# Kernel optimization log

Hardware: AMD Instinct MI355X
Metric: run time of the kernel (lower is better)

## Reference

```python
import jax, jax.numpy as jnp
import numpy as np

N, E = 50000, 800000
C, H, EC = 64, 3, 32  # node_channels, heads, edge_channels
NEG_SLOPE = 0.2


def _kaiming(key, shape, fan_in):
    bound = np.sqrt(6.0 / fan_in)  # kaiming_uniform_ default (a=sqrt(5)-ish approx; gain sqrt(2) variant)
    return jax.random.uniform(key, shape, jnp.float32, -bound, bound)


def setup_inputs() -> dict:
    key = jax.random.key(0)
    ks = jax.random.split(key, 8)
    x = jax.random.normal(ks[0], (N, C), jnp.float32)
    edge_index = jax.random.randint(ks[1], (2, E), 0, N, jnp.int64)
    edge_attr = jax.random.normal(ks[2], (E, EC), jnp.float32)
    weight_node = _kaiming(ks[3], (C, H * C), C)
    weight_edge = _kaiming(ks[4], (EC, H * C), EC)
    weight_triplet_att = _kaiming(ks[5], (1, H, 3 * C), 3 * C)
    weight_scale = _kaiming(ks[6], (H * C, C), H * C)
    bias = jnp.zeros((C,), jnp.float32)
    return {"x": x, "edge_index": edge_index, "edge_attr": edge_attr,
            "weight_node": weight_node, "weight_edge": weight_edge,
            "weight_triplet_att": weight_triplet_att,
            "weight_scale": weight_scale, "bias": bias}


def reference(x, edge_index, edge_attr, weight_node, weight_edge,
              weight_triplet_att, weight_scale, bias):
    src = edge_index[0]  # j (source)
    dst = edge_index[1]  # i (target), PyG default flow source_to_target

    xp = x @ weight_node                     # [N, H*C]
    ep = edge_attr @ weight_edge             # [E, H*C]

    x_j = xp[src].reshape(E, H, C)
    x_i = xp[dst].reshape(E, H, C)
    e_ij = ep.reshape(E, H, C)

    # attention weight split along concat order [x_i, e_ij, x_j]
    w = weight_triplet_att.reshape(H, 3, C)
    alpha = (jnp.einsum('ehc,hc->eh', x_i, w[:, 0])
             + jnp.einsum('ehc,hc->eh', e_ij, w[:, 1])
             + jnp.einsum('ehc,hc->eh', x_j, w[:, 2]))   # [E, H]
    alpha = jnp.where(alpha >= 0, alpha, NEG_SLOPE * alpha)  # leaky_relu

    # segment softmax over destination nodes (PyG softmax semantics)
    seg_max = jax.ops.segment_max(alpha, dst, num_segments=N)    # [N, H]
    alpha = jnp.exp(alpha - seg_max[dst])
    seg_sum = jax.ops.segment_sum(alpha, dst, num_segments=N)    # [N, H]
    alpha = alpha / (seg_sum[dst] + 1e-16)

    msg = alpha[:, :, None] * e_ij * x_j                         # [E, H, C]
    aggr = jax.ops.segment_sum(msg.reshape(E, H * C), dst, num_segments=N)  # [N, H*C]

    return aggr @ weight_scale + bias                            # [N, C]
```

## Files before the change

### kernel.cpp

```cpp
#include <hip/hip_runtime.h>

#define CC    64
#define HH    3
#define ECC   32
#define HCdim 192
#define NEG_SLOPE 0.2f
#define ASHIFT 12.0f
#define LOG2E  1.44269504f

typedef float v2f __attribute__((ext_vector_type(2)));

__global__ void tm_k0(const float* __restrict__ We, const float* __restrict__ wt,
                      float* __restrict__ u) {
    int t = threadIdx.x;
    if (t >= HH * ECC) return;
    int h = t >> 5, k = t & 31;
    float s = 0.f;
    #pragma unroll
    for (int c = 0; c < CC; ++c)
        s = fmaf(We[k * HCdim + h * CC + c], wt[h * HCdim + CC + c], s);
    u[t] = s;
}

#define K1_ROWS 64
__global__ __launch_bounds__(192) void tm_k1(const float* __restrict__ x,
        const float* __restrict__ Wn, const float* __restrict__ wt,
        const int* __restrict__ ei, int* __restrict__ deg,
        _Float16* __restrict__ xp16, float* __restrict__ sA, int N, int E) {
    __shared__ float wl[CC * HCdim];
    __shared__ float xl[K1_ROWS * CC];
    const int t = threadIdx.x;
    for (int i = blockIdx.x * 192 + t; i < E; i += gridDim.x * 192)
        atomicAdd(&deg[ei[E + i]], 1);
    const int h = t >> 6, c = t & 63;
    {
        float4* wl4 = (float4*)wl;
        const float4* Wn4 = (const float4*)Wn;
        for (int i = t; i < CC * HCdim / 4; i += 192) wl4[i] = Wn4[i];
    }
    const int base = blockIdx.x * K1_ROWS;
    const int rows = min(K1_ROWS, N - base);
    {
        float4* xl4 = (float4*)xl;
        const float4* x4 = (const float4*)(x + (size_t)base * CC);
        for (int i = t; i < rows * CC / 4; i += 192) xl4[i] = x4[i];
    }
    const float w0c = wt[h * HCdim + c];
    const float w2c = wt[h * HCdim + 2 * CC + c];
    __syncthreads();
    for (int rt = 0; rt < rows; rt += 4) {
        float acc0 = 0.f, acc1 = 0.f, acc2 = 0.f, acc3 = 0.f;
        #pragma unroll 4
        for (int k = 0; k < CC; k += 4) {
            const float w0  = wl[(k + 0) * HCdim + t];
            const float w1  = wl[(k + 1) * HCdim + t];
            const float w2_ = wl[(k + 2) * HCdim + t];
            const float w3  = wl[(k + 3) * HCdim + t];
            const float4 xa = *(const float4*)&xl[(rt + 0) * CC + k];
            const float4 xb = *(const float4*)&xl[(rt + 1) * CC + k];
            const float4 xc = *(const float4*)&xl[(rt + 2) * CC + k];
            const float4 xd = *(const float4*)&xl[(rt + 3) * CC + k];
            acc0 = fmaf(xa.x, w0, fmaf(xa.y, w1, fmaf(xa.z, w2_, fmaf(xa.w, w3, acc0))));
            acc1 = fmaf(xb.x, w0, fmaf(xb.y, w1, fmaf(xb.z, w2_, fmaf(xb.w, w3, acc1))));
            acc2 = fmaf(xc.x, w0, fmaf(xc.y, w1, fmaf(xc.z, w2_, fmaf(xc.w, w3, acc2))));
            acc3 = fmaf(xd.x, w0, fmaf(xd.y, w1, fmaf(xd.z, w2_, fmaf(xd.w, w3, acc3))));
        }
        #pragma unroll
        for (int r = 0; r < 4; ++r) {
            const float v = (r == 0) ? acc0 : (r == 1) ? acc1 : (r == 2) ? acc2 : acc3;
            const int n = base + rt + r;
            xp16[(size_t)n * HCdim + t] = (_Float16)v;
            float a0 = v * w0c, a2 = v * w2c;
            #pragma unroll
            for (int o = 32; o; o >>= 1) {
                a0 += __shfl_xor(a0, o);
                a2 += __shfl_xor(a2, o);
            }
            if (c == 0) {
                sA[n * 8 + h]     = a0;
                sA[n * 8 + 4 + h] = a2;
            }
        }
    }
}

__global__ __launch_bounds__(256) void tm_scanA(const int* __restrict__ deg,
        int* __restrict__ bsum, int N) {
    __shared__ int sd[256];
    int t = threadIdx.x, n = blockIdx.x * 256 + t;
    sd[t] = (n < N) ? deg[n] : 0;
    __syncthreads();
    for (int o = 128; o; o >>= 1) {
        if (t < o) sd[t] += sd[t + o];
        __syncthreads();
    }
    if (!t) bsum[blockIdx.x] = sd[0];
}

__global__ __launch_bounds__(256) void tm_scanB(const int* __restrict__ bsum,
        int* __restrict__ boff, int nb) {
    __shared__ int sd[256];
    int t = threadIdx.x;
    int v = (t < nb) ? bsum[t] : 0;
    sd[t] = v;
    __syncthreads();
    for (int o = 1; o < 256; o <<= 1) {
        int x = (t >= o) ? sd[t - o] : 0;
        __syncthreads();
        sd[t] += x;
        __syncthreads();
    }
    if (t < nb) boff[t] = sd[t] - v;
}

__global__ __launch_bounds__(256) void tm_scanC(const int* __restrict__ deg,
        const int* __restrict__ boff, int* __restrict__ off,
        int* __restrict__ cursor, int N) {
    __shared__ int sd[256];
    int t = threadIdx.x, n = blockIdx.x * 256 + t;
    int v = (n < N) ? deg[n] : 0;
    sd[t] = v;
    __syncthreads();
    for (int o = 1; o < 256; o <<= 1) {
        int x = (t >= o) ? sd[t - o] : 0;
        __syncthreads();
        sd[t] += x;
        __syncthreads();
    }
    if (n < N) {
        int ex = boff[blockIdx.x] + sd[t] - v;
        off[n] = ex;
        cursor[n] = ex;
        if (n == N - 1) off[N] = ex + v;
    }
}

__global__ __launch_bounds__(256) void tm_alpha(const int* __restrict__ ei,
        const float* __restrict__ ea, const float* __restrict__ u,
        const float* __restrict__ sA, int* __restrict__ cursor,
        float4* __restrict__ alphaE, int2* __restrict__ perm, int E) {
    __shared__ float ul[HH * ECC];
    const int t = threadIdx.x;
    if (t < HH * ECC) ul[t] = u[t];
    __syncthreads();
    const int e = blockIdx.x * 256 + t;
    if (e >= E) return;
    const int src = ei[e];
    const int dst = ei[E + e];
    float av[ECC];
    const float4* p4 = (const float4*)(ea + (size_t)e * ECC);
    #pragma unroll
    for (int q = 0; q < 8; ++q) {
        float4 v = p4[q];
        av[4*q] = v.x; av[4*q+1] = v.y; av[4*q+2] = v.z; av[4*q+3] = v.w;
    }
    float d0 = 0.f, d1 = 0.f, d2 = 0.f;
    #pragma unroll
    for (int k = 0; k < ECC; ++k) {
        d0 = fmaf(av[k], ul[k], d0);
        d1 = fmaf(av[k], ul[ECC + k], d1);
        d2 = fmaf(av[k], ul[2 * ECC + k], d2);
    }
    const float4 s0 = *(const float4*)(sA + (size_t)dst * 8);
    const float4 s2 = *(const float4*)(sA + (size_t)src * 8 + 4);
    float a0 = s0.x + d0 + s2.x;
    float a1 = s0.y + d1 + s2.y;
    float a2 = s0.z + d2 + s2.z;
    a0 = (a0 >= 0.f) ? a0 : NEG_SLOPE * a0;
    a1 = (a1 >= 0.f) ? a1 : NEG_SLOPE * a1;
    a2 = (a2 >= 0.f) ? a2 : NEG_SLOPE * a2;
    alphaE[e] = make_float4((a0 - ASHIFT) * LOG2E,
                            (a1 - ASHIFT) * LOG2E,
                            (a2 - ASHIFT) * LOG2E, 0.f);
    const int pos = atomicAdd(&cursor[dst], 1);
    perm[pos] = make_int2(src * (HCdim * 2), e * (ECC * 4));
}

__global__ __launch_bounds__(192) void tm_agg(const int2* __restrict__ perm,
        const int* __restrict__ off, const float* __restrict__ ea,
        const float* __restrict__ We, const float* __restrict__ alphaE,
        const _Float16* __restrict__ xp16, float* __restrict__ aggrN, int N) {
    const int t = threadIdx.x;
    const int h = t >> 6, lane = t & 63;
    const char* __restrict__ ea_b = (const char*)ea;
    const char* __restrict__ xp_b = (const char*)xp16;
    const char* __restrict__ al_b = (const char*)alphaE;
    v2f wcol2[16];
    #pragma unroll
    for (int k2 = 0; k2 < 16; ++k2) {
        wcol2[k2].x = We[(2 * k2)     * HCdim + h * CC + lane];
        wcol2[k2].y = We[(2 * k2 + 1) * HCdim + h * CC + lane];
    }
    const int xoff = h * (CC * 2) + lane * 2;
    const int aoff = h * 4;
    for (int n = blockIdx.x; n < N; n += gridDim.x) {
        const int start = off[n], end = off[n + 1];
        float s = 0.f, acc = 0.f;
        int pos = start;
        int4 pp = (pos + 2 <= end) ? *(const int4*)&perm[pos]
                                   : make_int4(0, 0, 0, 0);
        for (; pos + 2 <= end; ) {
            const int4 cur = pp;
            pos += 2;
            if (pos + 2 <= end) pp = *(const int4*)&perm[pos];
            const int so0 = __builtin_amdgcn_readfirstlane(cur.x);
            const int eo0 = __builtin_amdgcn_readfirstlane(cur.y);
            const int so1 = __builtin_amdgcn_readfirstlane(cur.z);
            const int eo1 = __builtin_amdgcn_readfirstlane(cur.w);
            const float a0 = *(const float*)(al_b + (eo0 >> 3) + aoff);
            const float a1 = *(const float*)(al_b + (eo1 >> 3) + aoff);
            const float4* q0 = (const float4*)(ea_b + eo0);
            const float4* q1 = (const float4*)(ea_b + eo1);
            const float xj0 = (float)*(const _Float16*)(xp_b + so0 + xoff);
            const float xj1 = (float)*(const _Float16*)(xp_b + so1 + xoff);
            v2f d0 = {0.f, 0.f}, d1 = {0.f, 0.f};
            #pragma unroll
            for (int q = 0; q < 8; ++q) {
                const float4 v0 = q0[q];
                const float4 v1 = q1[q];
                const v2f wlo = wcol2[2 * q], whi = wcol2[2 * q + 1];
                d0 = (v2f){v0.x, v0.y} * wlo + d0;
                d0 = (v2f){v0.z, v0.w} * whi + d0;
                d1 = (v2f){v1.x, v1.y} * wlo + d1;
                d1 = (v2f){v1.z, v1.w} * whi + d1;
            }
            const float p0 = exp2f(a0);
            const float p1 = exp2f(a1);
            s += p0 + p1;
            acc = fmaf(p0 * (d0.x + d0.y), xj0, acc);
            acc = fmaf(p1 * (d1.x + d1.y), xj1, acc);
        }
        if (pos < end) {
            const int2 pe = perm[pos];
            const int so = __builtin_amdgcn_readfirstlane(pe.x);
            const int eo = __builtin_amdgcn_readfirstlane(pe.y);
            const float a = *(const float*)(al_b + (eo >> 3) + aoff);
            const float4* q4 = (const float4*)(ea_b + eo);
            const float xj = (float)*(const _Float16*)(xp_b + so + xoff);
            v2f d = {0.f, 0.f};
            #pragma unroll
            for (int q = 0; q < 8; ++q) {
                const float4 v = q4[q];
                d = (v2f){v.x, v.y} * wcol2[2 * q]     + d;
                d = (v2f){v.z, v.w} * wcol2[2 * q + 1] + d;
            }
            const float p = exp2f(a);
            s += p;
            acc = fmaf(p * (d.x + d.y), xj, acc);
        }
        aggrN[(size_t)n * HCdim + h * CC + lane] = acc / (s + 1e-16f);
    }
}

#define K5_ROWS 16
__global__ __launch_bounds__(256) void tm_k5(const float* __restrict__ aggrN,
        const float* __restrict__ Ws, const float* __restrict__ bias,
        float* __restrict__ out, int N) {
    __shared__ float wsl[HCdim * CC];
    __shared__ float al[K5_ROWS * HCdim];
    const int t = threadIdx.x;
    const int part = t >> 6, c = t & 63;
    {
        float4* w4 = (float4*)wsl;
        const float4* Ws4 = (const float4*)Ws;
        for (int i = t; i < HCdim * CC / 4; i += 256) w4[i] = Ws4[i];
    }
    const float b = bias[c];
    const int base = blockIdx.x * K5_ROWS;
    const int rows = min(K5_ROWS, N - base);
    {
        float4* al4 = (float4*)al;
        const float4* a4 = (const float4*)(aggrN + (size_t)base * HCdim);
        for (int i = t; i < rows * HCdim / 4; i += 256) al4[i] = a4[i];
    }
    __syncthreads();
    const int r0 = part * 4;
    if (r0 >= rows) return;
    float acc0 = b, acc1 = b, acc2 = b, acc3 = b;
    #pragma unroll 4
    for (int k = 0; k < HCdim; k += 4) {
        const float w0  = wsl[(k + 0) * CC + c];
        const float w1  = wsl[(k + 1) * CC + c];
        const float w2_ = wsl[(k + 2) * CC + c];
        const float w3  = wsl[(k + 3) * CC + c];
        const float4 xa = *(const float4*)&al[(r0 + 0) * HCdim + k];
        const float4 xb = *(const float4*)&al[(r0 + 1) * HCdim + k];
        const float4 xc = *(const float4*)&al[(r0 + 2) * HCdim + k];
        const float4 xd = *(const float4*)&al[(r0 + 3) * HCdim + k];
        acc0 = fmaf(xa.x, w0, fmaf(xa.y, w1, fmaf(xa.z, w2_, fmaf(xa.w, w3, acc0))));
        acc1 = fmaf(xb.x, w0, fmaf(xb.y, w1, fmaf(xb.z, w2_, fmaf(xb.w, w3, acc1))));
        acc2 = fmaf(xc.x, w0, fmaf(xc.y, w1, fmaf(xc.z, w2_, fmaf(xc.w, w3, acc2))));
        acc3 = fmaf(xd.x, w0, fmaf(xd.y, w1, fmaf(xd.z, w2_, fmaf(xd.w, w3, acc3))));
    }
    if (r0 + 0 < rows) out[(size_t)(base + r0 + 0) * CC + c] = acc0;
    if (r0 + 1 < rows) out[(size_t)(base + r0 + 1) * CC + c] = acc1;
    if (r0 + 2 < rows) out[(size_t)(base + r0 + 2) * CC + c] = acc2;
    if (r0 + 3 < rows) out[(size_t)(base + r0 + 3) * CC + c] = acc3;
}

extern "C" void kernel_launch(void* const* d_in, const int* in_sizes, int n_in,
                              void* d_out, int out_size, void* d_ws, size_t ws_size,
                              hipStream_t stream) {
    const float* x    = (const float*)d_in[0];
    const int*   ei   = (const int*)d_in[1];
    const float* ea   = (const float*)d_in[2];
    const float* Wn   = (const float*)d_in[3];
    const float* We   = (const float*)d_in[4];
    const float* wt   = (const float*)d_in[5];
    const float* Ws   = (const float*)d_in[6];
    const float* bias = (const float*)d_in[7];
    float* out = (float*)d_out;
    const int N = in_sizes[0] / CC;
    const int E = in_sizes[1] / 2;
    const int nb = (N + 255) / 256;

    float* ws = (float*)d_ws;
    size_t o = 0;
    _Float16* xp16 = (_Float16*)(ws + o); o += (size_t)N * HCdim / 2;
    float* sA = ws + o;                  o += (size_t)N * 8;
    float* u  = ws + o;                  o += 128;
    float4* alphaE = (float4*)(ws + o);  o += (size_t)E * 4;
    int2*  perm = (int2*)(ws + o);       o += (size_t)E * 2 + 32;
    int* deg    = (int*)(ws + o);        o += N;
    int* off    = (int*)(ws + o);        o += N + 1;
    int* cursor = (int*)(ws + o);        o += N;
    int* bsum   = (int*)(ws + o);        o += 256;
    int* boff   = (int*)(ws + o);        o += 256;
    o += (4 - (o & 3)) & 3;
    float* aggrN = ws + o;               o += (size_t)N * HCdim;
    (void)ws_size; (void)n_in; (void)out_size;

    (void)hipMemsetAsync(deg, 0, (size_t)N * sizeof(int), stream);

    tm_k0<<<1, 96, 0, stream>>>(We, wt, u);
    tm_k1<<<(N + K1_ROWS - 1) / K1_ROWS, 192, 0, stream>>>(x, Wn, wt, ei, deg,
                                                           xp16, sA, N, E);
    tm_scanA<<<nb, 256, 0, stream>>>(deg, bsum, N);
    tm_scanB<<<1, 256, 0, stream>>>(bsum, boff, nb);
    tm_scanC<<<nb, 256, 0, stream>>>(deg, boff, off, cursor, N);
    tm_alpha<<<(E + 255) / 256, 256, 0, stream>>>(ei, ea, u, sA, cursor,
                                                  alphaE, perm, E);
    tm_agg<<<(N + 7) / 8, 192, 0, stream>>>(perm, off, ea, We,
                                            (const float*)alphaE, xp16, aggrN, N);
    tm_k5<<<(N + K5_ROWS - 1) / K5_ROWS, 256, 0, stream>>>(aggrN, Ws, bias, out, N);
}
```

Baseline: 423.6 us.

## Process all three heads per wave in aggregation kernel to reuse edge loads

```diff
diff --git a/kernel.cpp b/kernel.cpp
--- a/kernel.cpp
+++ b/kernel.cpp
@@ -176,79 +176,63 @@
     perm[pos] = make_int2(src * (HCdim * 2), e * (ECC * 4));
 }
 
-__global__ __launch_bounds__(192) void tm_agg(const int2* __restrict__ perm,
+__global__ __launch_bounds__(256) void tm_agg(const int2* __restrict__ perm,
         const int* __restrict__ off, const float* __restrict__ ea,
         const float* __restrict__ We, const float* __restrict__ alphaE,
         const _Float16* __restrict__ xp16, float* __restrict__ aggrN, int N) {
     const int t = threadIdx.x;
-    const int h = t >> 6, lane = t & 63;
+    const int wv = t >> 6, lane = t & 63;
     const char* __restrict__ ea_b = (const char*)ea;
     const char* __restrict__ xp_b = (const char*)xp16;
     const char* __restrict__ al_b = (const char*)alphaE;
-    v2f wcol2[16];
+    v2f wcol2[HH][16];
     #pragma unroll
-    for (int k2 = 0; k2 < 16; ++k2) {
-        wcol2[k2].x = We[(2 * k2)     * HCdim + h * CC + lane];
-        wcol2[k2].y = We[(2 * k2 + 1) * HCdim + h * CC + lane];
-    }
-    const int xoff = h * (CC * 2) + lane * 2;
-    const int aoff = h * 4;
-    for (int n = blockIdx.x; n < N; n += gridDim.x) {
+    for (int h = 0; h < HH; ++h)
+        #pragma unroll
+        for (int k2 = 0; k2 < 16; ++k2) {
+            wcol2[h][k2].x = We[(2 * k2)     * HCdim + h * CC + lane];
+            wcol2[h][k2].y = We[(2 * k2 + 1) * HCdim + h * CC + lane];
+        }
+    for (int n = blockIdx.x * 4 + wv; n < N; n += gridDim.x * 4) {
         const int start = off[n], end = off[n + 1];
-        float s = 0.f, acc = 0.f;
-        int pos = start;
-        int4 pp = (pos + 2 <= end) ? *(const int4*)&perm[pos]
-                                   : make_int4(0, 0, 0, 0);
-        for (; pos + 2 <= end; ) {
-            const int4 cur = pp;
-            pos += 2;
-            if (pos + 2 <= end) pp = *(const int4*)&perm[pos];
-            const int so0 = __builtin_amdgcn_readfirstlane(cur.x);
-            const int eo0 = __builtin_amdgcn_readfirstlane(cur.y);
-            const int so1 = __builtin_amdgcn_readfirstlane(cur.z);
-            const int eo1 = __builtin_amdgcn_readfirstlane(cur.w);
-            const float a0 = *(const float*)(al_b + (eo0 >> 3) + aoff);
-            const float a1 = *(const float*)(al_b + (eo1 >> 3) + aoff);
-            const float4* q0 = (const float4*)(ea_b + eo0);
-            const float4* q1 = (const float4*)(ea_b + eo1);
-            const float xj0 = (float)*(const _Float16*)(xp_b + so0 + xoff);
-            const float xj1 = (float)*(const _Float16*)(xp_b + so1 + xoff);
-            v2f d0 = {0.f, 0.f}, d1 = {0.f, 0.f};
-            #pragma unroll
-            for (int q = 0; q < 8; ++q) {
-                const float4 v0 = q0[q];
-                const float4 v1 = q1[q];
-                const v2f wlo = wcol2[2 * q], whi = wcol2[2 * q + 1];
-                d0 = (v2f){v0.x, v0.y} * wlo + d0;
-                d0 = (v2f){v0.z, v0.w} * whi + d0;
-                d1 = (v2f){v1.x, v1.y} * wlo + d1;
-                d1 = (v2f){v1.z, v1.w} * whi + d1;
-            }
-            const float p0 = exp2f(a0);
-            const float p1 = exp2f(a1);
-            s += p0 + p1;
-            acc = fmaf(p0 * (d0.x + d0.y), xj0, acc);
-            acc = fmaf(p1 * (d1.x + d1.y), xj1, acc);
-        }
-        if (pos < end) {
-            const int2 pe = perm[pos];
-            const int so = __builtin_amdgcn_readfirstlane(pe.x);
-            const int eo = __builtin_amdgcn_readfirstlane(pe.y);
-            const float a = *(const float*)(al_b + (eo >> 3) + aoff);
+        float s0 = 0.f, s1 = 0.f, s2 = 0.f;
+        float ac0 = 0.f, ac1 = 0.f, ac2 = 0.f;
+        int2 pe = (start < end) ? perm[start] : make_int2(0, 0);
+        for (int pos = start; pos < end; ++pos) {
+            const int2 cur = pe;
+            if (pos + 1 < end) pe = perm[pos + 1];
+            const int so = __builtin_amdgcn_readfirstlane(cur.x);
+            const int eo = __builtin_amdgcn_readfirstlane(cur.y);
+            const float4 av = *(const float4*)(al_b + (eo >> 3));
             const float4* q4 = (const float4*)(ea_b + eo);
-            const float xj = (float)*(const _Float16*)(xp_b + so + xoff);
-            v2f d = {0.f, 0.f};
+            const _Float16* xr = (const _Float16*)(xp_b + so) + lane;
+            const float xj0 = (float)xr[0];
+            const float xj1 = (float)xr[CC];
+            const float xj2 = (float)xr[2 * CC];
+            v2f d0 = {0.f, 0.f}, d1 = {0.f, 0.f}, d2 = {0.f, 0.f};
             #pragma unroll
             for (int q = 0; q < 8; ++q) {
                 const float4 v = q4[q];
-                d = (v2f){v.x, v.y} * wcol2[2 * q]     + d;
-                d = (v2f){v.z, v.w} * wcol2[2 * q + 1] + d;
+                const v2f lo = {v.x, v.y}, hi = {v.z, v.w};
+                d0 = lo * wcol2[0][2 * q]     + d0;
+                d0 = hi * wcol2[0][2 * q + 1] + d0;
+                d1 = lo * wcol2[1][2 * q]     + d1;
+                d1 = hi * wcol2[1][2 * q + 1] + d1;
+                d2 = lo * wcol2[2][2 * q]     + d2;
+                d2 = hi * wcol2[2][2 * q + 1] + d2;
             }
-            const float p = exp2f(a);
-            s += p;
-            acc = fmaf(p * (d.x + d.y), xj, acc);
+            const float p0 = exp2f(av.x);
+            const float p1 = exp2f(av.y);
+            const float p2 = exp2f(av.z);
+            s0 += p0; s1 += p1; s2 += p2;
+            ac0 = fmaf(p0 * (d0.x + d0.y), xj0, ac0);
+            ac1 = fmaf(p1 * (d1.x + d1.y), xj1, ac1);
+            ac2 = fmaf(p2 * (d2.x + d2.y), xj2, ac2);
         }
-        aggrN[(size_t)n * HCdim + h * CC + lane] = acc / (s + 1e-16f);
+        float* dstp = aggrN + (size_t)n * HCdim + lane;
+        dstp[0]      = ac0 / (s0 + 1e-16f);
+        dstp[CC]     = ac1 / (s1 + 1e-16f);
+        dstp[2 * CC] = ac2 / (s2 + 1e-16f);
     }
 }
 
@@ -340,7 +324,7 @@
     tm_scanC<<<nb, 256, 0, stream>>>(deg, boff, off, cursor, N);
     tm_alpha<<<(E + 255) / 256, 256, 0, stream>>>(ei, ea, u, sA, cursor,
                                                   alphaE, perm, E);
-    tm_agg<<<(N + 7) / 8, 192, 0, stream>>>(perm, off, ea, We,
-                                            (const float*)alphaE, xp16, aggrN, N);
+    tm_agg<<<(N + 31) / 32, 256, 0, stream>>>(perm, off, ea, We,
+                                              (const float*)alphaE, xp16, aggrN, N);
     tm_k5<<<(N + K5_ROWS - 1) / K5_ROWS, 256, 0, stream>>>(aggrN, Ws, bias, out, N);
 }
```

Result: slower. 439.4 us (+3.7%).
